# Performance work log

Hardware: AMD Instinct MI355X
Metric: run time of the kernel (lower is better)

## Reference

```python
import jax, jax.numpy as jnp
import numpy as np

BEAM = 10; MAX_LEN = 32; PAD = 1; BOS = 2; EOS = 3
NEG = jnp.float32(-1e30)


def lstm_cell(x, h, c, Wih, Whh, bih, bhh):
    # PyTorch LSTMCell gate order: i, f, g, o
    gates = x @ Wih.T + bih + h @ Whh.T + bhh
    i, f, g, o = jnp.split(gates, 4, axis=-1)
    c2 = jax.nn.sigmoid(f) * c + jax.nn.sigmoid(i) * jnp.tanh(g)
    h2 = jax.nn.sigmoid(o) * jnp.tanh(c2)
    return h2, c2


def setup_inputs() -> dict:
    key = jax.random.key(0)
    ks = jax.random.split(key, 14)
    G, P, E, H, S = 1000, 50000, 500, 500, 32
    s = lambda k, shape: jax.random.normal(k, shape, jnp.float32) * 0.05
    return {
        "g_seq": jax.random.randint(ks[0], (S, 1), 0, G),
        "enc_emb": s(ks[1], (G, E)),
        "enc_Wih": s(ks[2], (4 * H, E)), "enc_Whh": s(ks[3], (4 * H, H)),
        "enc_bih": s(ks[4], (4 * H,)), "enc_bhh": s(ks[5], (4 * H,)),
        "dec_emb": s(ks[6], (P, E)),
        "dec_Wih": s(ks[7], (4 * H, E)), "dec_Whh": s(ks[8], (4 * H, H)),
        "dec_bih": s(ks[9], (4 * H,)), "dec_bhh": s(ks[10], (4 * H,)),
        "attn_W": s(ks[11], (H, 2 * H)),
        "out_W": s(ks[12], (P, H)),
        "out_b": s(ks[13], (P,)),
    }


def reference(g_seq, enc_emb, enc_Wih, enc_Whh, enc_bih, enc_bhh,
              dec_emb, dec_Wih, dec_Whh, dec_bih, dec_bhh,
              attn_W, out_W, out_b):
    S = g_seq.shape[0]
    H = enc_Whh.shape[1]
    P = out_W.shape[0]

    # ---- encoder: unidirectional LSTMCell over seq, batch = 1 ----
    e_seq = enc_emb[g_seq[:, 0]]  # (S, E)
    def enc_step(carry, e):
        h, c = carry
        h, c = lstm_cell(e[None, :], h, c, enc_Wih, enc_Whh, enc_bih, enc_bhh)
        return (h, c), h[0]
    h0 = jnp.zeros((1, H), jnp.float32)
    (h, c), outs = jax.lax.scan(enc_step, (h0, h0), e_seq)  # outs: (S, H)

    # expand encoder state / context to beam
    context = jnp.broadcast_to(outs[None, :, :], (BEAM, S, H))
    h = jnp.broadcast_to(h, (BEAM, H))
    c = jnp.broadcast_to(c, (BEAM, H))
    scores = jnp.zeros((BEAM,), jnp.float32)
    tokens = jnp.full((BEAM,), PAD, jnp.int32).at[0].set(BOS)
    row0 = (jnp.arange(BEAM)[:, None] == 0)  # first-step mask: only beam 0 valid

    # ---- beam-search decode loop (run full max_len; early-eos break omitted,
    #      see notes: with eos=3 it only changes output when eos tops beam 0) ----
    def dec_step(carry, t):
        h, c, scores, tokens = carry
        e = dec_emb[tokens]                                   # (BEAM, E)
        h2, c2 = lstm_cell(e, h, c, dec_Wih, dec_Whh, dec_bih, dec_bhh)
        # dot attention
        attn = jax.nn.softmax(jnp.einsum('bsh,bh->bs', context, h2), axis=1)
        wctx = jnp.einsum('bs,bsh->bh', attn, context)
        o = jnp.tanh(jnp.concatenate([h2, wctx], axis=1) @ attn_W.T)
        logp = jax.nn.log_softmax(o @ out_W.T + out_b, axis=1)  # (BEAM, P)
        # first step: only beam 0 participates (original uses workd_lk[0])
        beam_lk = jnp.where(t == 0,
                            jnp.where(row0, logp, NEG),
                            logp + scores[:, None])
        best, idx = jax.lax.top_k(beam_lk.reshape(-1), BEAM)
        prev_k = idx // P
        next_y = idx - prev_k * P
        return (h2[prev_k], c2[prev_k], best, next_y), (prev_k, next_y)

    (_, _, scores, _), (prevKs, nextYs) = jax.lax.scan(
        dec_step, (h, c, scores, tokens), jnp.arange(MAX_LEN))

    # ---- hypothesis traceback, vectorized over beams ----
    def tb_step(k, t):
        tok = nextYs[t][k]
        return prevKs[t][k], tok
    _, toks = jax.lax.scan(tb_step, jnp.arange(BEAM), jnp.arange(MAX_LEN - 1, -1, -1))
    hyps = toks[::-1].T  # (BEAM, MAX_LEN)
    return hyps
```

## Files before the change

### kernel.cpp

```cpp
#include <hip/hip_runtime.h>
#include <math.h>

#define BEAM   10
#define MAXLEN 32
#define SLEN   32
#define HD     500
#define ED     500
#define G4     2000
#define PV     50000
#define NEGF   (-1e30f)
#define NEGD   (-1.0e30)

#define NSTRIP 196
#define CPR    (NSTRIP * BEAM)

typedef unsigned long long u64;

#define OFF_X      0
#define OFF_CBUF   64000
#define OFF_GBUF   65000
#define OFF_CTX    69000
#define OFF_DH     85000
#define OFF_DC     90000
#define OFF_DG     95000
#define OFF_H2     115000
#define OFF_C2     120000
#define OFF_O      125000
#define OFF_SCD    135000
#define OFF_TOK    135040
#define OFF_PREVK  135060
#define OFF_NEXTY  135380
#define OFF_PARTF  136000
#define OFF_CANDF  152000
#define OFF_LOG    160000
#define OFF_PARTD  160284
#define OFF_CAND   165604
#define OFF_OWT    660000
#define NEED_T_BYTES ((size_t)(OFF_OWT + (size_t)HD * PV) * 4)

__device__ __forceinline__ float sigf(float x) { return 1.f / (1.f + expf(-x)); }

__device__ __forceinline__ unsigned fkey(float f) {
    unsigned u = __float_as_uint(f);
    return (u & 0x80000000u) ? ~u : (u | 0x80000000u);
}
__device__ __forceinline__ float unfkey(unsigned k) {
    unsigned u = (k & 0x80000000u) ? (k & 0x7fffffffu) : ~k;
    return __uint_as_float(u);
}

__global__ void k_prep(const int* __restrict__ g_seq, const float* __restrict__ enc_emb,
                       const float* __restrict__ Wih, const float* __restrict__ bih,
                       const float* __restrict__ bhh, float* __restrict__ X,
                       float* __restrict__ cbuf0) {
    if (blockIdx.x == 0) {
        for (int j = threadIdx.x; j < HD; j += 256) cbuf0[j] = 0.f;
    }
    int wv = (blockIdx.x * blockDim.x + threadIdx.x) >> 6;
    int lane = threadIdx.x & 63;
    if (wv >= SLEN * G4) return;
    int t = wv / G4, r = wv - t * G4;
    const float* emb = enc_emb + (size_t)g_seq[t] * ED;
    const float* w = Wih + (size_t)r * ED;
    float acc = 0.f;
    for (int ki = 0; ki < 8; ki++) { int k = ki * 64 + lane; if (k < ED) acc += emb[k] * w[k]; }
    for (int o = 32; o; o >>= 1) acc += __shfl_down(acc, o);
    if (lane == 0) X[t * G4 + r] = acc + bih[r] + bhh[r];
}

__global__ void k_transpose4(const float* __restrict__ outW, float* __restrict__ outW4) {
    __shared__ float t_lds[64][65];
    int tid = threadIdx.x;
    int pbase = blockIdx.x * 64, kbase = blockIdx.y * 64;
    for (int e = 0; e < 16; e++) {
        int idx = e * 256 + tid; int pl = idx >> 6, kl = idx & 63;
        int pp = pbase + pl, kk = kbase + kl;
        t_lds[pl][kl] = (pp < PV && kk < HD) ? outW[(size_t)pp * HD + kk] : 0.f;
    }
    __syncthreads();
    for (int e = 0; e < 4; e++) {
        int idx = e * 256 + tid;
        int pl = idx & 63, kb = idx >> 6;
        int pp = pbase + pl;
        int kglob = kbase + kb * 4;
        if (pp < PV && kglob < HD) {
            float4 v;
            v.x = t_lds[pl][kb * 4 + 0];
            v.y = t_lds[pl][kb * 4 + 1];
            v.z = t_lds[pl][kb * 4 + 2];
            v.w = t_lds[pl][kb * 4 + 3];
            *(float4*)(outW4 + ((size_t)(kbase / 4 + kb) * PV + pp) * 4) = v;
        }
    }
}

__global__ void k_enc(const float* __restrict__ Whh, const float* __restrict__ X,
                      float* __restrict__ gbuf, float* __restrict__ cbuf,
                      float* __restrict__ context, float* __restrict__ dec_h,
                      float* __restrict__ dec_c, double* __restrict__ scores,
                      int* __restrict__ tokens, int t) {
    __shared__ float h_lds[HD];
    const float* gprev = gbuf + ((t + 1) & 1) * G4;
    float*       gcur  = gbuf + (t & 1) * G4;
    const float* cprev = cbuf + ((t + 1) & 1) * HD;
    float*       ccur  = cbuf + (t & 1) * HD;
    int tid = threadIdx.x;
    if (t > 0) {
        for (int j = tid; j < HD; j += 256) {
            float gi = gprev[j], gf = gprev[HD + j], gg = gprev[2 * HD + j], go = gprev[3 * HD + j];
            float c = sigf(gf) * cprev[j] + sigf(gi) * tanhf(gg);
            float h = sigf(go) * tanhf(c);
            h_lds[j] = h;
            if (blockIdx.x == 0) {
                ccur[j] = c;
                context[(t - 1) * HD + j] = h;
                if (t == SLEN) {
                    for (int b = 0; b < BEAM; b++) { dec_h[b * HD + j] = h; dec_c[b * HD + j] = c; }
                }
            }
        }
    } else {
        for (int j = tid; j < HD; j += 256) h_lds[j] = 0.f;
    }
    if (t == SLEN && blockIdx.x == 0 && tid == 0) {
        for (int b = 0; b < BEAM; b++) scores[b] = 0.0;
        tokens[0] = 2; for (int b = 1; b < BEAM; b++) tokens[b] = 1;
    }
    __syncthreads();
    if (t < SLEN) {
        int wv = blockIdx.x * 4 + (tid >> 6), lane = tid & 63;
        for (int r = wv; r < G4; r += 1000) {
            const float* w = Whh + (size_t)r * HD;
            float acc = 0.f;
            for (int ki = 0; ki < 8; ki++) { int k = ki * 64 + lane; if (k < HD) acc += h_lds[k] * w[k]; }
            for (int o = 32; o; o >>= 1) acc += __shfl_down(acc, o);
            if (lane == 0) gcur[r] = X[t * G4 + r] + acc;
        }
    }
}

struct MrgSm {
    double lse[BEAM]; double scl[BEAM];
    u64 rc[BEAM * BEAM];
    double gbv[8]; unsigned gbf[8]; unsigned winf;
    int pk[BEAM]; int ny[BEAM]; double val[BEAM];
};

__device__ __forceinline__ void do_merge(MrgSm* M, const double* __restrict__ part,
                                         const u64* __restrict__ cand,
                                         const double* __restrict__ sc_in,
                                         int m, int tid) {
    int wv = tid >> 6, lane = tid & 63;
    if (tid < BEAM) M->scl[tid] = sc_in[tid];
    for (int r = wv; r < BEAM; r += 8) {
        double s = 0.0;
        for (int i = lane; i < NSTRIP; i += 64) s += part[r * NSTRIP + i];
        for (int o = 32; o; o >>= 1) s += __shfl_down(s, o);
        if (lane == 0) M->lse[r] = log(s);
    }
    for (int r = wv; r < BEAM; r += 8) {
        u64 kk[31];
#pragma unroll
        for (int e = 0; e < 31; e++) {
            int i = lane + e * 64;
            kk[e] = (i < CPR) ? cand[(size_t)r * CPR + i] : 0ull;
        }
        for (int round = 0; round < BEAM; ++round) {
            u64 mx = 0ull;
#pragma unroll
            for (int e = 0; e < 31; e++) if (kk[e] > mx) mx = kk[e];
            for (int o = 32; o; o >>= 1) { u64 t2 = __shfl_down(mx, o); if (t2 > mx) mx = t2; }
            u64 win = __shfl(mx, 0);
#pragma unroll
            for (int e = 0; e < 31; e++) if (kk[e] == win) kk[e] = 0ull;
            if (lane == 0) M->rc[r * BEAM + round] = win;
        }
    }
    __syncthreads();
    double cv = -1.0e308; unsigned cf = 0xFFFFFFFFu;
    if (tid < BEAM * BEAM) {
        u64 k0 = M->rc[tid];
        if (k0) {
            int r2 = tid / BEAM;
            float v = unfkey((unsigned)(k0 >> 32));
            unsigned p = ~((unsigned)k0);
            double v2;
            if (m == 0) v2 = (r2 == 0) ? ((double)v - M->lse[0]) : NEGD;
            else        v2 = ((double)v - M->lse[r2]) + M->scl[r2];
            cv = v2; cf = (unsigned)r2 * PV + p;
        }
    }
    for (int round = 0; round < BEAM; ++round) {
        double bv = cv; unsigned bf = cf;
        for (int o = 32; o; o >>= 1) {
            double ov = __shfl_down(bv, o);
            unsigned of = __shfl_down(bf, o);
            if (ov > bv || (ov == bv && of < bf)) { bv = ov; bf = of; }
        }
        if (lane == 0) { M->gbv[wv] = bv; M->gbf[wv] = bf; }
        __syncthreads();
        if (tid == 0) {
            double xv = M->gbv[0]; unsigned xf = M->gbf[0];
            for (int i = 1; i < 8; i++) {
                if (M->gbv[i] > xv || (M->gbv[i] == xv && M->gbf[i] < xf)) { xv = M->gbv[i]; xf = M->gbf[i]; }
            }
            M->winf = xf;
            int pk = (int)(xf / PV);
            int ny = (int)(xf - (unsigned)pk * PV);
            M->pk[round] = pk; M->ny[round] = ny; M->val[round] = xv;
        }
        __syncthreads();
        if (cf == M->winf) { cv = -1.0e308; cf = 0xFFFFFFFFu; }
        __syncthreads();
    }
}

__global__ __launch_bounds__(512) void k_gates_m(
        const float* __restrict__ decEmb, const float* __restrict__ Wih,
        const float* __restrict__ Whh, const float* __restrict__ bih,
        const float* __restrict__ bhh,
        const double* __restrict__ part, const u64* __restrict__ cand,
        const double* __restrict__ sc_in, double* __restrict__ sc_out,
        const float* __restrict__ h2w, const float* __restrict__ c2w,
        float* __restrict__ dc, const float* __restrict__ dh0,
        int* __restrict__ prevK, int* __restrict__ nextY,
        float* __restrict__ gates, int t) {
    __shared__ float e_lds[BEAM * ED];
    __shared__ float h_lds[BEAM * HD];
    __shared__ MrgSm M;
    int tid = threadIdx.x, bid = blockIdx.x;
    int wv = tid >> 6, lane = tid & 63;

    if (t > 0) {
        int m = t - 1;
        do_merge(&M, part, cand, sc_in, m, tid);
        if (tid < BEAM && bid == 0) {
            sc_out[tid] = M.val[tid];
            prevK[m * BEAM + tid] = M.pk[tid];
            nextY[m * BEAM + tid] = M.ny[tid];
        }
        __syncthreads();
        for (int idx = tid; idx < BEAM * HD; idx += 512) {
            int b = idx / HD, j = idx - b * HD;
            h_lds[idx] = h2w[M.pk[b] * HD + j];
            e_lds[idx] = decEmb[(size_t)M.ny[b] * ED + j];
            if (bid == 0) dc[idx] = c2w[M.pk[b] * HD + j];
        }
    } else {
        for (int idx = tid; idx < BEAM * HD; idx += 512) {
            int b = idx / HD, j = idx - b * HD;
            int tk = (b == 0) ? 2 : 1;
            h_lds[idx] = dh0[idx];
            e_lds[idx] = decEmb[(size_t)tk * ED + j];
        }
    }
    __syncthreads();

    for (int rr = 0; rr < 2; ++rr) {
        int r = bid * 16 + wv * 2 + rr;
        const float* wi = Wih + (size_t)r * ED;
        const float* wh = Whh + (size_t)r * HD;
        float acc[BEAM];
#pragma unroll
        for (int b = 0; b < BEAM; b++) acc[b] = 0.f;
        for (int ki = 0; ki < 8; ki++) {
            int k = ki * 64 + lane;
            if (k < ED) {
                float w = wi[k];
#pragma unroll
                for (int b = 0; b < BEAM; b++) acc[b] += w * e_lds[b * ED + k];
            }
        }
        for (int ki = 0; ki < 8; ki++) {
            int k = ki * 64 + lane;
            if (k < HD) {
                float w = wh[k];
#pragma unroll
                for (int b = 0; b < BEAM; b++) acc[b] += w * h_lds[b * HD + k];
            }
        }
#pragma unroll
        for (int b = 0; b < BEAM; b++) {
            float v = acc[b];
            for (int o = 32; o; o >>= 1) v += __shfl_down(v, o);
            acc[b] = v;
        }
        if (lane == 0) {
            float bb = bih[r] + bhh[r];
#pragma unroll
            for (int b = 0; b < BEAM; b++) gates[b * G4 + r] = acc[b] + bb;
        }
    }
}

__global__ __launch_bounds__(256) void k_attn_oproj(
        const float* __restrict__ gates, const float* __restrict__ c_ws,
        const float* __restrict__ context, const float* __restrict__ attnW,
        float* __restrict__ h2_ws, float* __restrict__ c2_ws, float* __restrict__ o_ws) {
    __shared__ float h2_lds[BEAM * HD];
    __shared__ float wctx_lds[BEAM * HD];
    __shared__ float s_lds[BEAM * SLEN];
    __shared__ float a_lds[BEAM * SLEN];
    int tid = threadIdx.x;
    int wv = tid >> 6, lane = tid & 63;
    for (int idx = tid; idx < BEAM * HD; idx += 256) {
        int b = idx / HD, j = idx - b * HD;
        float gi = gates[b * G4 + j], gf = gates[b * G4 + HD + j];
        float gg = gates[b * G4 + 2 * HD + j], go = gates[b * G4 + 3 * HD + j];
        float c = sigf(gf) * c_ws[idx] + sigf(gi) * tanhf(gg);
        float h2 = sigf(go) * tanhf(c);
        h2_lds[idx] = h2;
        if (blockIdx.x == 0) { c2_ws[idx] = c; h2_ws[idx] = h2; }
    }
    __syncthreads();
    for (int si = 0; si < 8; ++si) {
        int s = wv + 4 * si;
        float acc[BEAM];
#pragma unroll
        for (int b = 0; b < BEAM; b++) acc[b] = 0.f;
        for (int ki = 0; ki < 8; ki++) {
            int k = ki * 64 + lane;
            if (k < HD) {
                float c = context[s * HD + k];
#pragma unroll
                for (int b = 0; b < BEAM; b++) acc[b] += c * h2_lds[b * HD + k];
            }
        }
#pragma unroll
        for (int b = 0; b < BEAM; b++) {
            float v = acc[b];
            for (int o = 32; o; o >>= 1) v += __shfl_down(v, o);
            if (lane == 0) s_lds[b * SLEN + s] = v;
        }
    }
    __syncthreads();
    if (wv == 0) {
        for (int b = 0; b < BEAM; ++b) {
            float v = (lane < SLEN) ? s_lds[b * SLEN + lane] : -INFINITY;
            float m = v;
            for (int o = 32; o; o >>= 1) m = fmaxf(m, __shfl_xor(m, o));
            float e = (lane < SLEN) ? expf(v - m) : 0.f;
            float sum = e;
            for (int o = 32; o; o >>= 1) sum += __shfl_xor(sum, o);
            if (lane < SLEN) a_lds[b * SLEN + lane] = e / sum;
        }
    }
    __syncthreads();
    {
        float w0[BEAM], w1[BEAM];
#pragma unroll
        for (int b = 0; b < BEAM; b++) { w0[b] = 0.f; w1[b] = 0.f; }
        int j0 = tid, j1 = tid + 256;
        for (int s = 0; s < SLEN; ++s) {
            float c0 = (j0 < HD) ? context[s * HD + j0] : 0.f;
            float c1 = (j1 < HD) ? context[s * HD + j1] : 0.f;
#pragma unroll
            for (int b = 0; b < BEAM; b++) {
                float a = a_lds[b * SLEN + s];
                w0[b] += a * c0; w1[b] += a * c1;
            }
        }
#pragma unroll
        for (int b = 0; b < BEAM; b++) {
            if (j0 < HD) wctx_lds[b * HD + j0] = w0[b];
            if (j1 < HD) wctx_lds[b * HD + j1] = w1[b];
        }
    }
    __syncthreads();
    int j = blockIdx.x * 4 + wv;
    const float* w = attnW + (size_t)j * 1000;
    float acc[BEAM];
#pragma unroll
    for (int b = 0; b < BEAM; b++) acc[b] = 0.f;
    for (int ki = 0; ki < 16; ki++) {
        int k = ki * 64 + lane;
        if (k < 1000) {
            float wk = w[k];
#pragma unroll
            for (int b = 0; b < BEAM; b++) {
                float h = (k < HD) ? h2_lds[b * HD + k] : wctx_lds[b * HD + k - HD];
                acc[b] += wk * h;
            }
        }
    }
#pragma unroll
    for (int b = 0; b < BEAM; b++) {
        float v = acc[b];
        for (int o = 32; o; o >>= 1) v += __shfl_down(v, o);
        acc[b] = v;
    }
    if (lane == 0) {
#pragma unroll
        for (int b = 0; b < BEAM; b++) o_ws[b * HD + j] = tanhf(acc[b]);
    }
}

__global__ __launch_bounds__(1024) void k_logits_topk(
        const float* __restrict__ outW4, const float* __restrict__ outB,
        const float* __restrict__ o_ws, u64* __restrict__ cand,
        double* __restrict__ part) {
    __shared__ __align__(16) char sm[61440];
    float4* o4 = (float4*)sm;
    float*  pt = (float*)(sm + 20480);
    int tid = threadIdx.x, bid = blockIdx.x;
    int lane = tid & 63;
    int col = tid & 255, kc = tid >> 8;
    for (int idx = tid; idx < BEAM * 125; idx += 1024) {
        int b = idx / 125, kb = idx - b * 125;
        o4[idx] = *(const float4*)(o_ws + b * HD + kb * 4);
    }
    __syncthreads();
    int p = bid * 256 + col;
    bool valid = (p < PV);
    int pc = valid ? p : (PV - 1);
    {
        float acc[BEAM];
#pragma unroll
        for (int b = 0; b < BEAM; b++) acc[b] = 0.f;
        int kb0 = kc * 32, kb1 = (kc == 3) ? 125 : (kb0 + 32);
        const float4* wp = (const float4*)outW4;
        for (int kb = kb0; kb < kb1; ++kb) {
            float4 w = wp[(size_t)kb * PV + pc];
#pragma unroll
            for (int b = 0; b < BEAM; b++) {
                float4 o = o4[b * 125 + kb];
                acc[b] += w.x * o.x + w.y * o.y + w.z * o.z + w.w * o.w;
            }
        }
#pragma unroll
        for (int b = 0; b < BEAM; b++) pt[(kc * 256 + col) * BEAM + b] = acc[b];
    }
    __syncthreads();
    float lg[BEAM];
    if (tid < 256) {
        float ob = outB[pc];
#pragma unroll
        for (int b = 0; b < BEAM; b++)
            lg[b] = pt[(0 * 256 + tid) * BEAM + b] + pt[(1 * 256 + tid) * BEAM + b]
                  + pt[(2 * 256 + tid) * BEAM + b] + pt[(3 * 256 + tid) * BEAM + b] + ob;
    }
    __syncthreads();
    double* pd = (double*)sm;
    u64*    kl = (u64*)(sm + 20480);
    if (tid < 256) {
#pragma unroll
        for (int b = 0; b < BEAM; b++) {
            pd[b * 256 + tid] = valid ? exp((double)lg[b]) : 0.0;
            kl[b * 256 + tid] = valid ? (((u64)fkey(lg[b]) << 32) | (unsigned)(~(unsigned)p)) : 0ull;
        }
    }
    __syncthreads();
    int wv = tid >> 6;
    if (wv < BEAM) {
        int r = wv;
        double s = pd[r * 256 + lane] + pd[r * 256 + 64 + lane]
                 + pd[r * 256 + 128 + lane] + pd[r * 256 + 192 + lane];
        for (int o = 32; o; o >>= 1) s += __shfl_down(s, o);
        if (lane == 0) part[r * NSTRIP + bid] = s;
        u64 kk[4];
#pragma unroll
        for (int j = 0; j < 4; j++) kk[j] = kl[r * 256 + j * 64 + lane];
        for (int round = 0; round < BEAM; round++) {
            u64 m = kk[0];
            if (kk[1] > m) m = kk[1];
            if (kk[2] > m) m = kk[2];
            if (kk[3] > m) m = kk[3];
            for (int o = 32; o; o >>= 1) {
                u64 t2 = __shfl_down(m, o);
                if (t2 > m) m = t2;
            }
            u64 win = __shfl(m, 0);
#pragma unroll
            for (int j = 0; j < 4; j++) if (kk[j] == win) kk[j] = 0ull;
            if (lane == 0) cand[(size_t)r * CPR + bid * 10 + round] = win;
        }
    }
}

__global__ __launch_bounds__(512) void k_final(
        const double* __restrict__ part, const u64* __restrict__ cand,
        const double* __restrict__ sc_in,
        int* __restrict__ prevK, int* __restrict__ nextY, int* __restrict__ out) {
    __shared__ MrgSm M;
    int tid = threadIdx.x;
    do_merge(&M, part, cand, sc_in, MAXLEN - 1, tid);
    if (tid < BEAM) {
        prevK[(MAXLEN - 1) * BEAM + tid] = M.pk[tid];
        nextY[(MAXLEN - 1) * BEAM + tid] = M.ny[tid];
    }
    __syncthreads();
    if (tid < BEAM) {
        int cur = tid;
        for (int tt = MAXLEN - 1; tt >= 0; tt--) {
            out[tid * MAXLEN + tt] = nextY[tt * BEAM + cur];
            cur = prevK[tt * BEAM + cur];
        }
    }
}

__global__ __launch_bounds__(1024) void k_gates(
        const float* __restrict__ dec_emb, const float* __restrict__ Wih,
        const float* __restrict__ Whh, const float* __restrict__ bih,
        const float* __restrict__ bhh, const int* __restrict__ tokens,
        const float* __restrict__ h_ws, float* __restrict__ gates) {
    __shared__ float e_lds[BEAM * ED];
    __shared__ float h_lds[BEAM * HD];
    int tid = threadIdx.x;
    for (int idx = tid; idx < BEAM * ED; idx += 1024) {
        int b = idx / ED, k = idx - b * ED;
        e_lds[idx] = dec_emb[(size_t)tokens[b] * ED + k];
        h_lds[idx] = h_ws[idx];
    }
    __syncthreads();
    int wv = tid >> 6, lane = tid & 63;
    int r = blockIdx.x * 16 + wv;
    const float* wi = Wih + (size_t)r * ED;
    const float* wh = Whh + (size_t)r * HD;
    float acc[BEAM];
#pragma unroll
    for (int b = 0; b < BEAM; b++) acc[b] = 0.f;
    for (int ki = 0; ki < 8; ki++) {
        int k = ki * 64 + lane;
        if (k < ED) {
            float w = wi[k];
#pragma unroll
            for (int b = 0; b < BEAM; b++) acc[b] += w * e_lds[b * ED + k];
        }
    }
    for (int ki = 0; ki < 8; ki++) {
        int k = ki * 64 + lane;
        if (k < HD) {
            float w = wh[k];
#pragma unroll
            for (int b = 0; b < BEAM; b++) acc[b] += w * h_lds[b * HD + k];
        }
    }
#pragma unroll
    for (int b = 0; b < BEAM; b++) {
        float v = acc[b];
        for (int o = 32; o; o >>= 1) v += __shfl_down(v, o);
        acc[b] = v;
    }
    if (lane == 0) {
        float bb = bih[r] + bhh[r];
#pragma unroll
        for (int b = 0; b < BEAM; b++) gates[b * G4 + r] = acc[b] + bb;
    }
}

__global__ void k_logits_f(const float* __restrict__ outW, const float* __restrict__ outB,
                           const float* __restrict__ o_ws, float* __restrict__ logits,
                           double* __restrict__ partials) {
    __shared__ float o_lds[BEAM * HD];
    __shared__ double ered[4][BEAM];
    int tid = threadIdx.x;
    for (int idx = tid; idx < BEAM * HD; idx += 256) o_lds[idx] = o_ws[idx];
    __syncthreads();
    int wv = tid >> 6, lane = tid & 63;
    int w = blockIdx.x * 4 + wv;
    double esum = 0.0;
    for (int pi = 0; pi < 16; pi++) {
        int p = w * 16 + pi;
        if (p >= PV) break;
        const float* wr = outW + (size_t)p * HD;
        float acc[BEAM];
#pragma unroll
        for (int b = 0; b < BEAM; b++) acc[b] = 0.f;
        for (int ki = 0; ki < 8; ki++) {
            int k = ki * 64 + lane;
            if (k < HD) {
                float x = wr[k];
#pragma unroll
                for (int b = 0; b < BEAM; b++) acc[b] += x * o_lds[b * HD + k];
            }
        }
#pragma unroll
        for (int b = 0; b < BEAM; b++)
            for (int o = 32; o; o >>= 1) acc[b] += __shfl_xor(acc[b], o);
        if (lane < BEAM) {
            float lg = 0.f;
#pragma unroll
            for (int b = 0; b < BEAM; b++) if (lane == b) lg = acc[b];
            lg += outB[p];
            logits[(size_t)lane * PV + p] = lg;
            esum += exp((double)lg);
        }
    }
    if (lane < BEAM) ered[wv][lane] = esum;
    __syncthreads();
    if (tid < BEAM) partials[blockIdx.x * BEAM + tid] =
        ered[0][tid] + ered[1][tid] + ered[2][tid] + ered[3][tid];
}

__global__ __launch_bounds__(256) void k_topk_row(const float* __restrict__ logits,
                                                  u64* __restrict__ cands) {
    const int CH = 1563;
    int r = blockIdx.x >> 5, ci = blockIdx.x & 31;
    int base = ci * CH;
    int tid = threadIdx.x;
    int wv = tid >> 6, lane = tid & 63;
    u64 key[7];
#pragma unroll
    for (int e = 0; e < 7; e++) {
        int p = base + e * 256 + tid;
        key[e] = 0ull;
        if (p < base + CH && p < PV) {
            float v = logits[(size_t)r * PV + p];
            key[e] = ((u64)fkey(v) << 32) | (unsigned)(~(unsigned)p);
        }
    }
    __shared__ u64 wred[4];
    __shared__ u64 winlds;
    for (int round = 0; round < BEAM; round++) {
        u64 mx = 0ull;
#pragma unroll
        for (int e = 0; e < 7; e++) if (key[e] > mx) mx = key[e];
        for (int o = 32; o; o >>= 1) {
            u64 other = __shfl_down(mx, o);
            if (other > mx) mx = other;
        }
        if (lane == 0) wred[wv] = mx;
        __syncthreads();
        if (tid == 0) {
            u64 wn = wred[0];
            for (int i = 1; i < 4; i++) if (wred[i] > wn) wn = wred[i];
            winlds = wn;
            cands[blockIdx.x * BEAM + round] = wn;
        }
        __syncthreads();
        u64 win = winlds;
#pragma unroll
        for (int e = 0; e < 7; e++) if (key[e] == win) key[e] = 0ull;
    }
}

__global__ __launch_bounds__(256) void k_merge(
        const double* __restrict__ partials, int npart,
        const u64* __restrict__ cands,
        double* __restrict__ scores, int* __restrict__ tokens,
        const float* __restrict__ h2_ws, const float* __restrict__ c2_ws,
        float* __restrict__ h_ws, float* __restrict__ c_ws,
        int* __restrict__ prevKs, int* __restrict__ nextYs, int t) {
    __shared__ double wredd[4];
    __shared__ double lse_lds[BEAM];
    __shared__ double sc_lds[BEAM];
    __shared__ double bwv[4];
    __shared__ unsigned bwf[4];
    __shared__ unsigned winf_s;
    __shared__ int pk_lds[BEAM];
    __shared__ int ny_lds[BEAM];
    __shared__ double val_lds[BEAM];
    int tid = threadIdx.x;
    int wv = tid >> 6, lane = tid & 63;
    if (tid < BEAM) sc_lds[tid] = scores[tid];
    for (int b = 0; b < BEAM; b++) {
        double s = 0.0;
        for (int j = tid; j < npart; j += 256) s += partials[j * BEAM + b];
        for (int o = 32; o; o >>= 1) s += __shfl_down(s, o);
        if (lane == 0) wredd[wv] = s;
        __syncthreads();
        if (tid == 0) lse_lds[b] = log(wredd[0] + wredd[1] + wredd[2] + wredd[3]);
        __syncthreads();
    }
    double   cv[13];
    unsigned cf[13];
#pragma unroll
    for (int e = 0; e < 13; e++) {
        int c = e * 256 + tid;
        cv[e] = -1.0e308; cf[e] = 0xFFFFFFFFu;
        if (c < 3200) {
            u64 k0 = cands[c];
            if (k0) {
                int r = c / 320;
                float v = unfkey((unsigned)(k0 >> 32));
                unsigned p = ~((unsigned)k0);
                double v2;
                if (t == 0) v2 = (r == 0) ? ((double)v - lse_lds[0]) : (double)NEGF;
                else        v2 = ((double)v - lse_lds[r]) + sc_lds[r];
                cv[e] = v2;
                cf[e] = (unsigned)r * PV + p;
            }
        }
    }
    for (int round = 0; round < BEAM; round++) {
        double bv = -1.0e308; unsigned bf = 0xFFFFFFFFu;
#pragma unroll
        for (int e = 0; e < 13; e++) {
            if (cv[e] > bv || (cv[e] == bv && cf[e] < bf)) { bv = cv[e]; bf = cf[e]; }
        }
        for (int o = 32; o; o >>= 1) {
            double ov = __shfl_down(bv, o);
            unsigned of = __shfl_down(bf, o);
            if (ov > bv || (ov == bv && of < bf)) { bv = ov; bf = of; }
        }
        if (lane == 0) { bwv[wv] = bv; bwf[wv] = bf; }
        __syncthreads();
        if (tid == 0) {
            double xv = bwv[0]; unsigned xf = bwf[0];
            for (int i = 1; i < 4; i++) {
                if (bwv[i] > xv || (bwv[i] == xv && bwf[i] < xf)) { xv = bwv[i]; xf = bwf[i]; }
            }
            winf_s = xf;
            int pk = (int)(xf / PV);
            int ny = (int)(xf - (unsigned)pk * PV);
            pk_lds[round] = pk; ny_lds[round] = ny; val_lds[round] = xv;
        }
        __syncthreads();
        unsigned wff = winf_s;
#pragma unroll
        for (int e = 0; e < 13; e++) {
            if (cf[e] == wff) { cv[e] = -1.0e308; cf[e] = 0xFFFFFFFFu; }
        }
    }
    if (tid < BEAM) {
        scores[tid] = val_lds[tid];
        tokens[tid] = ny_lds[tid];
        prevKs[t * BEAM + tid] = pk_lds[tid];
        nextYs[t * BEAM + tid] = ny_lds[tid];
    }
    __syncthreads();
    for (int idx = tid; idx < BEAM * HD; idx += 256) {
        int i = idx / HD, j = idx - i * HD;
        h_ws[idx] = h2_ws[pk_lds[i] * HD + j];
        c_ws[idx] = c2_ws[pk_lds[i] * HD + j];
    }
}

__global__ void k_traceback(const int* __restrict__ prevKs, const int* __restrict__ nextYs,
                            int* __restrict__ out) {
    int k = threadIdx.x;
    if (k >= BEAM) return;
    int cur = k;
    for (int t = MAXLEN - 1; t >= 0; t--) {
        out[k * MAXLEN + t] = nextYs[t * BEAM + cur];
        cur = prevKs[t * BEAM + cur];
    }
}

extern "C" void kernel_launch(void* const* d_in, const int* in_sizes, int n_in,
                              void* d_out, int out_size, void* d_ws, size_t ws_size,
                              hipStream_t stream) {
    const int*   g_seq  = (const int*)  d_in[0];
    const float* encEmb = (const float*)d_in[1];
    const float* encWih = (const float*)d_in[2];
    const float* encWhh = (const float*)d_in[3];
    const float* encBih = (const float*)d_in[4];
    const float* encBhh = (const float*)d_in[5];
    const float* decEmb = (const float*)d_in[6];
    const float* decWih = (const float*)d_in[7];
    const float* decWhh = (const float*)d_in[8];
    const float* decBih = (const float*)d_in[9];
    const float* decBhh = (const float*)d_in[10];
    const float* attnW  = (const float*)d_in[11];
    const float* outW   = (const float*)d_in[12];
    const float* outB   = (const float*)d_in[13];

    float* ws = (float*)d_ws;
    float*  X     = ws + OFF_X;
    float*  cbuf  = ws + OFF_CBUF;
    float*  gbuf  = ws + OFF_GBUF;
    float*  ctx   = ws + OFF_CTX;
    float*  dh    = ws + OFF_DH;
    float*  dc    = ws + OFF_DC;
    float*  dg    = ws + OFF_DG;
    float*  h2    = ws + OFF_H2;
    float*  c2    = ws + OFF_C2;
    float*  o     = ws + OFF_O;
    double* scb   = (double*)(ws + OFF_SCD);
    int*    tok   = (int*)(ws + OFF_TOK);
    int*    prevK = (int*)(ws + OFF_PREVK);
    int*    nextY = (int*)(ws + OFF_NEXTY);
    float*  outW4 = ws + OFF_OWT;

    bool bigws = (ws_size >= NEED_T_BYTES);

    k_prep<<<16000, 256, 0, stream>>>(g_seq, encEmb, encWih, encBih, encBhh, X, cbuf);
    if (bigws) k_transpose4<<<dim3(782, 8), 256, 0, stream>>>(outW, outW4);

    for (int t = 0; t <= SLEN; t++)
        k_enc<<<250, 256, 0, stream>>>(encWhh, X, gbuf, cbuf, ctx, dh, dc, scb, tok, t);

    if (bigws) {
        double* part = (double*)(ws + OFF_PARTD);
        u64*    cand = (u64*)(ws + OFF_CAND);
        for (int t = 0; t < MAXLEN; t++) {
            int m = t - 1;
            const double* sin = scb + ((m & 1) ? 10 : 0);
            double*       sout = scb + (((m + 1) & 1) ? 10 : 0);
            if (t == 0) { sin = scb; sout = scb + 10; }
            k_gates_m<<<125, 512, 0, stream>>>(decEmb, decWih, decWhh, decBih, decBhh,
                                               part, cand, sin, sout,
                                               h2, c2, dc, dh, prevK, nextY, dg, t);
            k_attn_oproj<<<125, 256, 0, stream>>>(dg, dc, ctx, attnW, h2, c2, o);
            k_logits_topk<<<NSTRIP, 1024, 0, stream>>>(outW4, outB, o, cand, part);
        }
        int mf = MAXLEN - 1;
        k_final<<<1, 512, 0, stream>>>(part, cand, scb + ((mf & 1) ? 10 : 0),
                                       prevK, nextY, (int*)d_out);
    } else {
        double* part  = (double*)(ws + OFF_PARTF);
        u64*    cand  = (u64*)(ws + OFF_CANDF);
        float*  logits = ws + OFF_LOG;
        const int npart = 782;
        for (int t = 0; t < MAXLEN; t++) {
            k_gates<<<125, 1024, 0, stream>>>(decEmb, decWih, decWhh, decBih, decBhh, tok, dh, dg);
            k_attn_oproj<<<125, 256, 0, stream>>>(dg, dc, ctx, attnW, h2, c2, o);
            k_logits_f<<<782, 256, 0, stream>>>(outW, outB, o, logits, part);
            k_topk_row<<<320, 256, 0, stream>>>(logits, cand);
            k_merge<<<1, 256, 0, stream>>>(part, npart, cand, scb, tok, h2, c2, dh, dc, prevK, nextY, t);
        }
        k_traceback<<<1, 64, 0, stream>>>(prevK, nextY, (int*)d_out);
    }
}
```

Before: 4.010 ms.

## Fuse attention and output projection into logits/top-k kernel

```diff
diff --git a/kernel.cpp b/kernel.cpp
--- a/kernel.cpp
+++ b/kernel.cpp
@@ -293,6 +293,253 @@
     }
 }
 
+__global__ __launch_bounds__(1024) void k_fused(
+        const float* __restrict__ gates, const float* __restrict__ c_ws,
+        const float* __restrict__ context, const float* __restrict__ attnW,
+        float* __restrict__ h2_ws, float* __restrict__ c2_ws,
+        const float* __restrict__ outW4, const float* __restrict__ outB,
+        u64* __restrict__ cand, double* __restrict__ part) {
+    __shared__ __align__(16) char sm[62560];
+    float* h2_lds   = (float*)sm;
+    float* wctx_lds = (float*)(sm + 20000);
+    float* s_lds    = (float*)(sm + 40000);
+    float* a_lds    = (float*)(sm + 41280);
+    float* o_lds    = (float*)(sm + 42560);
+    int tid = threadIdx.x, bid = blockIdx.x;
+    int wv = tid >> 6, lane = tid & 63;
+
+    for (int idx = tid; idx < BEAM * HD; idx += 1024) {
+        int b = idx / HD, j = idx - b * HD;
+        float gi = gates[b * G4 + j], gf = gates[b * G4 + HD + j];
+        float gg = gates[b * G4 + 2 * HD + j], go = gates[b * G4 + 3 * HD + j];
+        float c = sigf(gf) * c_ws[idx] + sigf(gi) * tanhf(gg);
+        float h2 = sigf(go) * tanhf(c);
+        h2_lds[idx] = h2;
+        if (bid == 0) { c2_ws[idx] = c; h2_ws[idx] = h2; }
+    }
+    __syncthreads();
+
+    for (int si = 0; si < 2; ++si) {
+        int s = wv + 16 * si;
+        float acc[BEAM];
+#pragma unroll
+        for (int b = 0; b < BEAM; b++) acc[b] = 0.f;
+        for (int ki = 0; ki < 8; ki++) {
+            int k = ki * 64 + lane;
+            if (k < HD) {
+                float c = context[s * HD + k];
+#pragma unroll
+                for (int b = 0; b < BEAM; b++) acc[b] += c * h2_lds[b * HD + k];
+            }
+        }
+#pragma unroll
+        for (int b = 0; b < BEAM; b++) {
+            float v = acc[b];
+            for (int o = 32; o; o >>= 1) v += __shfl_down(v, o);
+            if (lane == 0) s_lds[b * SLEN + s] = v;
+        }
+    }
+    __syncthreads();
+
+    if (wv == 0) {
+        for (int b = 0; b < BEAM; ++b) {
+            float v = (lane < SLEN) ? s_lds[b * SLEN + lane] : -INFINITY;
+            float m = v;
+            for (int o = 32; o; o >>= 1) m = fmaxf(m, __shfl_xor(m, o));
+            float e = (lane < SLEN) ? expf(v - m) : 0.f;
+            float sum = e;
+            for (int o = 32; o; o >>= 1) sum += __shfl_xor(sum, o);
+            if (lane < SLEN) a_lds[b * SLEN + lane] = e / sum;
+        }
+    }
+    __syncthreads();
+
+    if (tid < HD) {
+        float w0[BEAM];
+#pragma unroll
+        for (int b = 0; b < BEAM; b++) w0[b] = 0.f;
+        for (int s = 0; s < SLEN; ++s) {
+            float c0 = context[s * HD + tid];
+#pragma unroll
+            for (int b = 0; b < BEAM; b++) w0[b] += a_lds[b * SLEN + s] * c0;
+        }
+#pragma unroll
+        for (int b = 0; b < BEAM; b++) wctx_lds[b * HD + tid] = w0[b];
+    }
+    __syncthreads();
+
+    for (int jj = 0; jj < 32; ++jj) {
+        int j = wv + 16 * jj;
+        if (j < HD) {
+            const float* w = attnW + (size_t)j * 1000;
+            float acc[BEAM];
+#pragma unroll
+            for (int b = 0; b < BEAM; b++) acc[b] = 0.f;
+            for (int ki = 0; ki < 16; ki++) {
+                int k = ki * 64 + lane;
+                if (k < 1000) {
+                    float wk = w[k];
+#pragma unroll
+                    for (int b = 0; b < BEAM; b++) {
+                        float h = (k < HD) ? h2_lds[b * HD + k] : wctx_lds[b * HD + k - HD];
+                        acc[b] += wk * h;
+                    }
+                }
+            }
+#pragma unroll
+            for (int b = 0; b < BEAM; b++) {
+                float v = acc[b];
+                for (int o = 32; o; o >>= 1) v += __shfl_down(v, o);
+                acc[b] = v;
+            }
+            if (lane == 0) {
+#pragma unroll
+                for (int b = 0; b < BEAM; b++) o_lds[b * HD + j] = tanhf(acc[b]);
+            }
+        }
+    }
+    __syncthreads();
+
+    float* pt = (float*)sm;
+    int col = tid & 255, kc = tid >> 8;
+    int p = bid * 256 + col;
+    bool valid = (p < PV);
+    int pc = valid ? p : (PV - 1);
+    {
+        float acc[BEAM];
+#pragma unroll
+        for (int b = 0; b < BEAM; b++) acc[b] = 0.f;
+        int kb0 = kc * 32, kb1 = (kc == 3) ? 125 : (kb0 + 32);
+        const float4* wp = (const float4*)outW4;
+        const float4* o4 = (const float4*)o_lds;
+        for (int kb = kb0; kb < kb1; ++kb) {
+            float4 w = wp[(size_t)kb * PV + pc];
+#pragma unroll
+            for (int b = 0; b < BEAM; b++) {
+                float4 o = o4[b * 125 + kb];
+                acc[b] += w.x * o.x + w.y * o.y + w.z * o.z + w.w * o.w;
+            }
+        }
+#pragma unroll
+        for (int b = 0; b < BEAM; b++) pt[(kc * 256 + col) * BEAM + b] = acc[b];
+    }
+    __syncthreads();
+    float lg[BEAM];
+    if (tid < 256) {
+        float ob = outB[pc];
+#pragma unroll
+        for (int b = 0; b < BEAM; b++)
+            lg[b] = pt[(0 * 256 + tid) * BEAM + b] + pt[(1 * 256 + tid) * BEAM + b]
+                  + pt[(2 * 256 + tid) * BEAM + b] + pt[(3 * 256 + tid) * BEAM + b] + ob;
+    }
+    __syncthreads();
+    double* pd = (double*)sm;
+    u64*    kl = (u64*)(sm + 20480);
+    if (tid < 256) {
+#pragma unroll
+        for (int b = 0; b < BEAM; b++) {
+            pd[b * 256 + tid] = valid ? exp((double)lg[b]) : 0.0;
+            kl[b * 256 + tid] = valid ? (((u64)fkey(lg[b]) << 32) | (unsigned)(~(unsigned)p)) : 0ull;
+        }
+    }
+    __syncthreads();
+    if (wv < BEAM) {
+        int r = wv;
+        double s = pd[r * 256 + lane] + pd[r * 256 + 64 + lane]
+                 + pd[r * 256 + 128 + lane] + pd[r * 256 + 192 + lane];
+        for (int o = 32; o; o >>= 1) s += __shfl_down(s, o);
+        if (lane == 0) part[r * NSTRIP + bid] = s;
+        u64 kk[4];
+#pragma unroll
+        for (int j = 0; j < 4; j++) kk[j] = kl[r * 256 + j * 64 + lane];
+        for (int round = 0; round < BEAM; round++) {
+            u64 m = kk[0];
+            if (kk[1] > m) m = kk[1];
+            if (kk[2] > m) m = kk[2];
+            if (kk[3] > m) m = kk[3];
+            for (int o = 32; o; o >>= 1) {
+                u64 t2 = __shfl_down(m, o);
+                if (t2 > m) m = t2;
+            }
+            u64 win = __shfl(m, 0);
+#pragma unroll
+            for (int j = 0; j < 4; j++) if (kk[j] == win) kk[j] = 0ull;
+            if (lane == 0) cand[(size_t)r * CPR + bid * 10 + round] = win;
+        }
+    }
+}
+
+__global__ __launch_bounds__(512) void k_final(
+        const double* __restrict__ part, const u64* __restrict__ cand,
+        const double* __restrict__ sc_in,
+        int* __restrict__ prevK, int* __restrict__ nextY, int* __restrict__ out) {
+    __shared__ MrgSm M;
+    int tid = threadIdx.x;
+    do_merge(&M, part, cand, sc_in, MAXLEN - 1, tid);
+    if (tid < BEAM) {
+        prevK[(MAXLEN - 1) * BEAM + tid] = M.pk[tid];
+        nextY[(MAXLEN - 1) * BEAM + tid] = M.ny[tid];
+    }
+    __syncthreads();
+    if (tid < BEAM) {
+        int cur = tid;
+        for (int tt = MAXLEN - 1; tt >= 0; tt--) {
+            out[tid * MAXLEN + tt] = nextY[tt * BEAM + cur];
+            cur = prevK[tt * BEAM + cur];
+        }
+    }
+}
+
+__global__ __launch_bounds__(1024) void k_gates(
+        const float* __restrict__ dec_emb, const float* __restrict__ Wih,
+        const float* __restrict__ Whh, const float* __restrict__ bih,
+        const float* __restrict__ bhh, const int* __restrict__ tokens,
+        const float* __restrict__ h_ws, float* __restrict__ gates) {
+    __shared__ float e_lds[BEAM * ED];
+    __shared__ float h_lds[BEAM * HD];
+    int tid = threadIdx.x;
+    for (int idx = tid; idx < BEAM * ED; idx += 1024) {
+        int b = idx / ED, k = idx - b * ED;
+        e_lds[idx] = dec_emb[(size_t)tokens[b] * ED + k];
+        h_lds[idx] = h_ws[idx];
+    }
+    __syncthreads();
+    int wv = tid >> 6, lane = tid & 63;
+    int r = blockIdx.x * 16 + wv;
+    const float* wi = Wih + (size_t)r * ED;
+    const float* wh = Whh + (size_t)r * HD;
+    float acc[BEAM];
+#pragma unroll
+    for (int b = 0; b < BEAM; b++) acc[b] = 0.f;
+    for (int ki = 0; ki < 8; ki++) {
+        int k = ki * 64 + lane;
+        if (k < ED) {
+            float w = wi[k];
+#pragma unroll
+            for (int b = 0; b < BEAM; b++) acc[b] += w * e_lds[b * ED + k];
+        }
+    }
+    for (int ki = 0; ki < 8; ki++) {
+        int k = ki * 64 + lane;
+        if (k < HD) {
+            float w = wh[k];
+#pragma unroll
+            for (int b = 0; b < BEAM; b++) acc[b] += w * h_lds[b * HD + k];
+        }
+    }
+#pragma unroll
+    for (int b = 0; b < BEAM; b++) {
+        float v = acc[b];
+        for (int o = 32; o; o >>= 1) v += __shfl_down(v, o);
+        acc[b] = v;
+    }
+    if (lane == 0) {
+        float bb = bih[r] + bhh[r];
+#pragma unroll
+        for (int b = 0; b < BEAM; b++) gates[b * G4 + r] = acc[b] + bb;
+    }
+}
+
 __global__ __launch_bounds__(256) void k_attn_oproj(
         const float* __restrict__ gates, const float* __restrict__ c_ws,
         const float* __restrict__ context, const float* __restrict__ attnW,
@@ -392,159 +639,6 @@
     if (lane == 0) {
 #pragma unroll
         for (int b = 0; b < BEAM; b++) o_ws[b * HD + j] = tanhf(acc[b]);
-    }
-}
-
-__global__ __launch_bounds__(1024) void k_logits_topk(
-        const float* __restrict__ outW4, const float* __restrict__ outB,
-        const float* __restrict__ o_ws, u64* __restrict__ cand,
-        double* __restrict__ part) {
-    __shared__ __align__(16) char sm[61440];
-    float4* o4 = (float4*)sm;
-    float*  pt = (float*)(sm + 20480);
-    int tid = threadIdx.x, bid = blockIdx.x;
-    int lane = tid & 63;
-    int col = tid & 255, kc = tid >> 8;
-    for (int idx = tid; idx < BEAM * 125; idx += 1024) {
-        int b = idx / 125, kb = idx - b * 125;
-        o4[idx] = *(const float4*)(o_ws + b * HD + kb * 4);
-    }
-    __syncthreads();
-    int p = bid * 256 + col;
-    bool valid = (p < PV);
-    int pc = valid ? p : (PV - 1);
-    {
-        float acc[BEAM];
-#pragma unroll
-        for (int b = 0; b < BEAM; b++) acc[b] = 0.f;
-        int kb0 = kc * 32, kb1 = (kc == 3) ? 125 : (kb0 + 32);
-        const float4* wp = (const float4*)outW4;
-        for (int kb = kb0; kb < kb1; ++kb) {
-            float4 w = wp[(size_t)kb * PV + pc];
-#pragma unroll
-            for (int b = 0; b < BEAM; b++) {
-                float4 o = o4[b * 125 + kb];
-                acc[b] += w.x * o.x + w.y * o.y + w.z * o.z + w.w * o.w;
-            }
-        }
-#pragma unroll
-        for (int b = 0; b < BEAM; b++) pt[(kc * 256 + col) * BEAM + b] = acc[b];
-    }
-    __syncthreads();
-    float lg[BEAM];
-    if (tid < 256) {
-        float ob = outB[pc];
-#pragma unroll
-        for (int b = 0; b < BEAM; b++)
-            lg[b] = pt[(0 * 256 + tid) * BEAM + b] + pt[(1 * 256 + tid) * BEAM + b]
-                  + pt[(2 * 256 + tid) * BEAM + b] + pt[(3 * 256 + tid) * BEAM + b] + ob;
-    }
-    __syncthreads();
-    double* pd = (double*)sm;
-    u64*    kl = (u64*)(sm + 20480);
-    if (tid < 256) {
-#pragma unroll
-        for (int b = 0; b < BEAM; b++) {
-            pd[b * 256 + tid] = valid ? exp((double)lg[b]) : 0.0;
-            kl[b * 256 + tid] = valid ? (((u64)fkey(lg[b]) << 32) | (unsigned)(~(unsigned)p)) : 0ull;
-        }
-    }
-    __syncthreads();
-    int wv = tid >> 6;
-    if (wv < BEAM) {
-        int r = wv;
-        double s = pd[r * 256 + lane] + pd[r * 256 + 64 + lane]
-                 + pd[r * 256 + 128 + lane] + pd[r * 256 + 192 + lane];
-        for (int o = 32; o; o >>= 1) s += __shfl_down(s, o);
-        if (lane == 0) part[r * NSTRIP + bid] = s;
-        u64 kk[4];
-#pragma unroll
-        for (int j = 0; j < 4; j++) kk[j] = kl[r * 256 + j * 64 + lane];
-        for (int round = 0; round < BEAM; round++) {
-            u64 m = kk[0];
-            if (kk[1] > m) m = kk[1];
-            if (kk[2] > m) m = kk[2];
-            if (kk[3] > m) m = kk[3];
-            for (int o = 32; o; o >>= 1) {
-                u64 t2 = __shfl_down(m, o);
-                if (t2 > m) m = t2;
-            }
-            u64 win = __shfl(m, 0);
-#pragma unroll
-            for (int j = 0; j < 4; j++) if (kk[j] == win) kk[j] = 0ull;
-            if (lane == 0) cand[(size_t)r * CPR + bid * 10 + round] = win;
-        }
-    }
-}
-
-__global__ __launch_bounds__(512) void k_final(
-        const double* __restrict__ part, const u64* __restrict__ cand,
-        const double* __restrict__ sc_in,
-        int* __restrict__ prevK, int* __restrict__ nextY, int* __restrict__ out) {
-    __shared__ MrgSm M;
-    int tid = threadIdx.x;
-    do_merge(&M, part, cand, sc_in, MAXLEN - 1, tid);
-    if (tid < BEAM) {
-        prevK[(MAXLEN - 1) * BEAM + tid] = M.pk[tid];
-        nextY[(MAXLEN - 1) * BEAM + tid] = M.ny[tid];
-    }
-    __syncthreads();
-    if (tid < BEAM) {
-        int cur = tid;
-        for (int tt = MAXLEN - 1; tt >= 0; tt--) {
-            out[tid * MAXLEN + tt] = nextY[tt * BEAM + cur];
-            cur = prevK[tt * BEAM + cur];
-        }
-    }
-}
-
-__global__ __launch_bounds__(1024) void k_gates(
-        const float* __restrict__ dec_emb, const float* __restrict__ Wih,
-        const float* __restrict__ Whh, const float* __restrict__ bih,
-        const float* __restrict__ bhh, const int* __restrict__ tokens,
-        const float* __restrict__ h_ws, float* __restrict__ gates) {
-    __shared__ float e_lds[BEAM * ED];
-    __shared__ float h_lds[BEAM * HD];
-    int tid = threadIdx.x;
-    for (int idx = tid; idx < BEAM * ED; idx += 1024) {
-        int b = idx / ED, k = idx - b * ED;
-        e_lds[idx] = dec_emb[(size_t)tokens[b] * ED + k];
-        h_lds[idx] = h_ws[idx];
-    }
-    __syncthreads();
-    int wv = tid >> 6, lane = tid & 63;
-    int r = blockIdx.x * 16 + wv;
-    const float* wi = Wih + (size_t)r * ED;
-    const float* wh = Whh + (size_t)r * HD;
-    float acc[BEAM];
-#pragma unroll
-    for (int b = 0; b < BEAM; b++) acc[b] = 0.f;
-    for (int ki = 0; ki < 8; ki++) {
-        int k = ki * 64 + lane;
-        if (k < ED) {
-            float w = wi[k];
-#pragma unroll
-            for (int b = 0; b < BEAM; b++) acc[b] += w * e_lds[b * ED + k];
-        }
-    }
-    for (int ki = 0; ki < 8; ki++) {
-        int k = ki * 64 + lane;
-        if (k < HD) {
-            float w = wh[k];
-#pragma unroll
-            for (int b = 0; b < BEAM; b++) acc[b] += w * h_lds[b * HD + k];
-        }
-    }
-#pragma unroll
-    for (int b = 0; b < BEAM; b++) {
-        float v = acc[b];
-        for (int o = 32; o; o >>= 1) v += __shfl_down(v, o);
-        acc[b] = v;
-    }
-    if (lane == 0) {
-        float bb = bih[r] + bhh[r];
-#pragma unroll
-        for (int b = 0; b < BEAM; b++) gates[b * G4 + r] = acc[b] + bb;
     }
 }
 
@@ -791,8 +885,8 @@
             k_gates_m<<<125, 512, 0, stream>>>(decEmb, decWih, decWhh, decBih, decBhh,
                                                part, cand, sin, sout,
                                                h2, c2, dc, dh, prevK, nextY, dg, t);
-            k_attn_oproj<<<125, 256, 0, stream>>>(dg, dc, ctx, attnW, h2, c2, o);
-            k_logits_topk<<<NSTRIP, 1024, 0, stream>>>(outW4, outB, o, cand, part);
+            k_fused<<<NSTRIP, 1024, 0, stream>>>(dg, dc, ctx, attnW, h2, c2,
+                                                 outW4, outB, cand, part);
         }
         int mf = MAXLEN - 1;
         k_final<<<1, 512, 0, stream>>>(part, cand, scb + ((mf & 1) ? 10 : 0),
```

Result: slower. 8.614 ms (+114.8%).
